# Kernel tuning notes

Measured on AMD Instinct MI355X. Metric: run time of the kernel, lower is better.

The kernel has to match this reference:

```python
import jax, jax.numpy as jnp
import numpy as np
from functools import partial

NPOINT, NSAMPLE = 1024, 32
EPS = 1e-5

def setup_inputs() -> dict:
    key = jax.random.key(0)
    ks = jax.random.split(key, 16)
    B, N, C = 16, 4096, 64
    d = {
        "xyz": jax.random.normal(ks[0], (B, N, 3), jnp.float32),
        "points": jax.random.normal(ks[1], (B, N, C), jnp.float32),
    }
    chans = [67, 64, 64, 128]
    for i in range(3):
        cin, cout = chans[i], chans[i + 1]
        d[f"w{i+1}"] = jax.random.normal(ks[2 + i], (cout, cin), jnp.float32) * (1.0 / np.sqrt(cin))
        d[f"b{i+1}"] = jnp.zeros((cout,), jnp.float32)
        d[f"g{i+1}"] = jnp.ones((cout,), jnp.float32)
        d[f"be{i+1}"] = jnp.zeros((cout,), jnp.float32)
    return d

def farthest_point_sample(xyz, npoint):
    # xyz: (B, N, 3); deterministic start index 0 (torch code uses randint)
    B, N, _ = xyz.shape
    bidx = jnp.arange(B)

    def step(carry, _):
        distance, farthest = carry
        centroid = xyz[bidx, farthest]                       # (B, 3)
        dist = jnp.sum((xyz - centroid[:, None, :]) ** 2, -1)  # (B, N)
        distance = jnp.minimum(distance, dist)
        return (distance, jnp.argmax(distance, axis=1)), farthest

    init = (jnp.full((B, N), 1e10, xyz.dtype), jnp.zeros((B,), jnp.int32))
    _, centroids = jax.lax.scan(step, init, None, length=npoint)  # (npoint, B)
    return centroids.T                                            # (B, npoint)

def knn_group(nsample, xyz, new_xyz, points):
    # xyz: (B,N,3), new_xyz: (B,S,3), points: (B,N,C)
    # squared distances (same topk ordering as cdist)
    d2 = (jnp.sum(new_xyz ** 2, -1)[:, :, None]
          + jnp.sum(xyz ** 2, -1)[:, None, :]
          - 2.0 * jnp.einsum("bsd,bnd->bsn", new_xyz, xyz))     # (B,S,N)
    _, idx = jax.lax.top_k(-d2, nsample)                          # (B,S,K)

    gather = jax.vmap(lambda feats, i: feats[i])                  # per-batch fancy index
    grouped_xyz = gather(xyz, idx) - new_xyz[:, :, None, :]       # (B,S,K,3)
    grouped_pts = jnp.concatenate([grouped_xyz, gather(points, idx)], -1)  # (B,S,K,3+C)
    return grouped_xyz, grouped_pts

def mlp_layer(x, w, b, g, be):
    # 1x1 conv + BatchNorm (batch stats, training mode) + ReLU
    y = jnp.einsum("bskc,oc->bsko", x, w) + b
    mu = jnp.mean(y, axis=(0, 1, 2))
    var = jnp.var(y, axis=(0, 1, 2))
    y = (y - mu) * jax.lax.rsqrt(var + EPS) * g + be
    return jax.nn.relu(y)

def reference(xyz, points, w1, b1, g1, be1, w2, b2, g2, be2, w3, b3, g3, be3):
    centroids = farthest_point_sample(xyz, NPOINT)                    # (B,S)
    new_xyz = jnp.take_along_axis(xyz, centroids[:, :, None], axis=1)  # (B,S,3)
    _, x = knn_group(NSAMPLE, xyz, new_xyz, points)                   # (B,S,K,3+C)
    x = mlp_layer(x, w1, b1, g1, be1)
    x = mlp_layer(x, w2, b2, g2, be2)
    x = mlp_layer(x, w3, b3, g3, be3)
    new_points = jnp.max(x, axis=2)                                   # (B,S,mlp[-1])
    return new_xyz, new_points
```

## Files before the change

### kernel.cpp

```cpp
#include <hip/hip_runtime.h>

typedef unsigned int   uint;
typedef unsigned short ushort;
typedef unsigned long long u64;
typedef float f32x4 __attribute__((ext_vector_type(4)));
typedef short bf16x8 __attribute__((ext_vector_type(8)));
typedef uint  uint2v __attribute__((ext_vector_type(2)));

#define STR 88

__device__ __forceinline__ uint packbf2(float a, float b){
  uint ua=__float_as_uint(a); ua=(ua+0x7fffu+((ua>>16)&1u))>>16;
  uint ub=__float_as_uint(b); ub=(ub+0x7fffu+((ub>>16)&1u))>>16;
  return ua|(ub<<16);
}
__device__ __forceinline__ ushort bf1(float a){
  uint ua=__float_as_uint(a); return (ushort)((ua+0x7fffu+((ua>>16)&1u))>>16);
}

__device__ __forceinline__ void dot16x2(const float* __restrict__ wr,
                                        const f32x4* xa, const f32x4* xb,
                                        float& accA, float& accB){
#pragma unroll
  for (int k=0;k<4;k++){
    f32x4 w=*(const f32x4*)(wr+4*k);
    accA=fmaf(xa[k][0],w[0],accA); accA=fmaf(xa[k][1],w[1],accA);
    accA=fmaf(xa[k][2],w[2],accA); accA=fmaf(xa[k][3],w[3],accA);
    accB=fmaf(xb[k][0],w[0],accB); accB=fmaf(xb[k][1],w[1],accB);
    accB=fmaf(xb[k][2],w[2],accB); accB=fmaf(xb[k][3],w[3],accB);
  }
}

__global__ __launch_bounds__(256) void k_fps(const float* __restrict__ xyz,
                                             int* __restrict__ cent,
                                             float* __restrict__ oxyz){
  __shared__ __align__(16) float sp[4096][4];
  __shared__ u64 rk[2][4];
  __shared__ int sel[1024];
  const int b = blockIdx.x, tid = threadIdx.x, lane=tid&63, wave=tid>>6;
  const float* xb = xyz + (long)b*4096*3;
  float px[16], py[16], pz[16], pd[16];
#pragma unroll
  for (int j=0;j<16;j++){
    int n = tid + 256*j;
    float x=xb[n*3], y=xb[n*3+1], z=xb[n*3+2];
    sp[n][0]=x; sp[n][1]=y; sp[n][2]=z; sp[n][3]=0.0f;
    px[j]=x; py[j]=y; pz[j]=z; pd[j]=1e10f;
  }
  if (tid==0) sel[0]=0;
  __syncthreads();
  int f = 0;
  for (int t=1;t<1024;t++){
    f32x4 c = *(const f32x4*)sp[f];
    float bv=-1.0f; int bi=0;
#pragma unroll
    for (int j=0;j<16;j++){
      int n = tid + 256*j;
      float dx=px[j]-c[0], dy=py[j]-c[1], dz=pz[j]-c[2];
      float d=__fadd_rn(__fadd_rn(__fmul_rn(dx,dx),__fmul_rn(dy,dy)),__fmul_rn(dz,dz));
      float mn=fminf(pd[j],d); pd[j]=mn;
      if (j==0){ bv=mn; bi=n; }
      else if (mn>bv){ bv=mn; bi=n; }
    }
    u64 key = ((u64)__float_as_uint(bv)<<32) | (uint)(~bi);
#pragma unroll
    for (int off=32;off;off>>=1){
      u64 ok=__shfl_xor(key,off);
      key = ok>key ? ok : key;
    }
    int par=t&1;
    if (lane==0) rk[par][wave]=key;
    __syncthreads();
    {
      u64 k0=rk[par][0], k1=rk[par][1], k2=rk[par][2], k3=rk[par][3];
      u64 ka = k0>k1?k0:k1;
      u64 kb = k2>k3?k2:k3;
      u64 kk = ka>kb?ka:kb;
      f = (int)(~(uint)kk) & 4095;
    }
    if (tid==0) sel[t]=f;
  }
  __syncthreads();
#pragma unroll
  for (int j=0;j<4;j++){
    int s = tid + 256*j;
    int n = sel[s];
    cent[b*1024+s]=n;
    f32x4 cf=*(const f32x4*)sp[n];
    oxyz[(b*1024+s)*3+0]=cf[0];
    oxyz[(b*1024+s)*3+1]=cf[1];
    oxyz[(b*1024+s)*3+2]=cf[2];
  }
}

__global__ __launch_bounds__(256) void k_knn(const float* __restrict__ xyz,
                                             const int* __restrict__ cent,
                                             ushort* __restrict__ kidx){
  __shared__ float sx[4096], sy[4096], sz[4096];
  const int bx=blockIdx.x, b=bx>>5, chunk=bx&31;
  const int tid=threadIdx.x, lane=tid&63, wave=tid>>6;
  const float* xb = xyz + (long)b*4096*3;
#pragma unroll
  for (int j=0;j<16;j++){
    int n = tid + 256*j;
    sx[n]=xb[n*3]; sy[n]=xb[n*3+1]; sz[n]=xb[n*3+2];
  }
  __syncthreads();
  const u64 SENT=~0ull;
  for (int qp=0; qp<4; qp++){
    int sA = chunk*32 + wave*8 + qp*2;
    int sB = sA + 1;
    int qnA = cent[b*1024 + sA] & 4095;
    int qnB = cent[b*1024 + sB] & 4095;
    double qxA=(double)sx[qnA], qyA=(double)sy[qnA], qzA=(double)sz[qnA];
    double qxB=(double)sx[qnB], qyB=(double)sy[qnB], qzB=(double)sz[qnB];
    u64 k1A=SENT, k2A=SENT, k1B=SENT, k2B=SENT;
#pragma unroll 4
    for (int j=0;j<64;j++){
      int n = lane + 64*j;
      double px=(double)sx[n], py=(double)sy[n], pz=(double)sz[n];
      double dxA=px-qxA, dyA=py-qyA, dzA=pz-qzA;
      double dxB=px-qxB, dyB=py-qyB, dzB=pz-qzB;
      double d2A = dxA*dxA + dyA*dyA + dzA*dzA;
      double d2B = dxB*dxB + dyB*dyB + dzB*dzB;
      u64 kdA = (((u64)__double_as_longlong(d2A)) & ~4095ull) | (uint)n;
      u64 kdB = (((u64)__double_as_longlong(d2B)) & ~4095ull) | (uint)n;
      if (kdA<k1A){ k2A=k1A; k1A=kdA; }
      else if (kdA<k2A){ k2A=kdA; }
      if (kdB<k1B){ k2B=k1B; k1B=kdB; }
      else if (kdB<k2B){ k2B=kdB; }
    }
    u64 removedA=0ull, removedB=0ull;
    ushort* outA = kidx + (b*1024 + sA)*32;
    ushort* outB = kidx + (b*1024 + sB)*32;
    for (int r=0;r<32;r++){
      u64 wkA=k1A, wkB=k1B;
#pragma unroll
      for (int off=32;off;off>>=1){
        u64 okA=__shfl_xor(wkA,off);
        u64 okB=__shfl_xor(wkB,off);
        wkA = okA<wkA ? okA : wkA;
        wkB = okB<wkB ? okB : wkB;
      }
      if (lane==0){ outA[r]=(ushort)(wkA & 4095u); outB[r]=(ushort)(wkB & 4095u); }
      if (wkA==k1A){
        removedA |= 1ull << (((uint)(k1A&4095u))>>6);
        if (k2A!=SENT){ k1A=k2A; k2A=SENT; }
        else {
          k1A=SENT; k2A=SENT;
#pragma unroll 4
          for (int j=0;j<64;j++){
            if ((removedA>>j)&1ull) continue;
            int n = lane + 64*j;
            double dx=(double)sx[n]-qxA, dy=(double)sy[n]-qyA, dz=(double)sz[n]-qzA;
            double d2 = dx*dx + dy*dy + dz*dz;
            u64 kd = (((u64)__double_as_longlong(d2)) & ~4095ull) | (uint)n;
            if (kd<k1A){ k2A=k1A; k1A=kd; }
            else if (kd<k2A){ k2A=kd; }
          }
        }
      }
      if (wkB==k1B){
        removedB |= 1ull << (((uint)(k1B&4095u))>>6);
        if (k2B!=SENT){ k1B=k2B; k2B=SENT; }
        else {
          k1B=SENT; k2B=SENT;
#pragma unroll 4
          for (int j=0;j<64;j++){
            if ((removedB>>j)&1ull) continue;
            int n = lane + 64*j;
            double dx=(double)sx[n]-qxB, dy=(double)sy[n]-qyB, dz=(double)sz[n]-qzB;
            double d2 = dx*dx + dy*dy + dz*dz;
            u64 kd = (((u64)__double_as_longlong(d2)) & ~4095ull) | (uint)n;
            if (kd<k1B){ k2B=k1B; k1B=kd; }
            else if (kd<k2B){ k2B=kd; }
          }
        }
      }
    }
  }
}

__global__ __launch_bounds__(256) void k_mlp1b(const float* __restrict__ xyz,
                                               const float* __restrict__ pts,
                                               const float* __restrict__ w1,
                                               const float* __restrict__ b1,
                                               const int* __restrict__ cent,
                                               const ushort* __restrict__ kidx,
                                               float* __restrict__ part,
                                               float* __restrict__ y){
  __shared__ __align__(16) float L[9760];
  float* W1  = L;
  float* XIN = L+4384;
  float* WRED= L+8736;
  const int tid=threadIdx.x, bi=blockIdx.x;
  const int row=tid>>3, oc=tid&7, wave=tid>>6;
  const int b=bi>>6, s0=(bi&63)*16;
  const long bN=(long)b*4096;

  for (int i=tid;i<64*68;i+=256){
    int r=i/68, c=i-r*68;
    float v = (c<64)? w1[r*67+3+c] : (c<67? w1[r*67+(c-64)] : 0.0f);
    W1[r*68+((r>>3)<<2)+c]=v;
  }
  float breg1[8];
#pragma unroll
  for (int i=0;i<8;i++) breg1[i]=b1[oc*8+i];
  float ps[8], pq[8];
#pragma unroll
  for (int s=0;s<8;s++){ ps[s]=0.f; pq[s]=0.f; }
  __syncthreads();

  for (int t=0; t<8; t++){
    int sgA = b*1024 + s0 + t*2, sgB = sgA+1;
    {
      int nA = kidx[sgA*32+row] & 4095;
      int nB = kidx[sgB*32+row] & 4095;
      const float* prA = pts + (bN+nA)*64;
      const float* prB = pts + (bN+nB)*64;
      *(f32x4*)(XIN + row*68 + oc*8)          = *(const f32x4*)(prA + oc*8);
      *(f32x4*)(XIN + row*68 + oc*8 + 4)      = *(const f32x4*)(prA + oc*8 + 4);
      *(f32x4*)(XIN + (row+32)*68 + oc*8)     = *(const f32x4*)(prB + oc*8);
      *(f32x4*)(XIN + (row+32)*68 + oc*8 + 4) = *(const f32x4*)(prB + oc*8 + 4);
      if (oc==0){
        int qA = cent[sgA] & 4095, qB = cent[sgB] & 4095;
        const float* xpA = xyz + (bN+nA)*3; const float* qpA = xyz + (bN+qA)*3;
        const float* xpB = xyz + (bN+nB)*3; const float* qpB = xyz + (bN+qB)*3;
        XIN[row*68+64]=xpA[0]-qpA[0]; XIN[row*68+65]=xpA[1]-qpA[1];
        XIN[row*68+66]=xpA[2]-qpA[2]; XIN[row*68+67]=0.0f;
        XIN[(row+32)*68+64]=xpB[0]-qpB[0]; XIN[(row+32)*68+65]=xpB[1]-qpB[1];
        XIN[(row+32)*68+66]=xpB[2]-qpB[2]; XIN[(row+32)*68+67]=0.0f;
      }
    }
    const float* xrowA = XIN + row*68;
    const float* xrowB = XIN + (row+32)*68;
    float acc[2][8];
#pragma unroll
    for (int i=0;i<8;i++){ acc[0][i]=breg1[i]; acc[1][i]=breg1[i]; }
#pragma unroll
    for (int co=0;co<4;co++){
      f32x4 xa[4], xbv[4];
#pragma unroll
      for (int k=0;k<4;k++){ xa[k]=*(const f32x4*)(xrowA+co*16+4*k); xbv[k]=*(const f32x4*)(xrowB+co*16+4*k); }
#pragma unroll
      for (int i=0;i<8;i++)
        dot16x2(W1+(oc*8+i)*68+(oc<<2)+co*16, xa, xbv, acc[0][i], acc[1][i]);
    }
    {
      f32x4 xtA=*(const f32x4*)(xrowA+64), xtB=*(const f32x4*)(xrowB+64);
#pragma unroll
      for (int i=0;i<8;i++){
        const float* wr=W1+(oc*8+i)*68+(oc<<2)+64;
        f32x4 w=*(const f32x4*)wr;
        acc[0][i]=fmaf(xtA[0],w[0],acc[0][i]); acc[0][i]=fmaf(xtA[1],w[1],acc[0][i]);
        acc[0][i]=fmaf(xtA[2],w[2],acc[0][i]); acc[0][i]=fmaf(xtA[3],w[3],acc[0][i]);
        acc[1][i]=fmaf(xtB[0],w[0],acc[1][i]); acc[1][i]=fmaf(xtB[1],w[1],acc[1][i]);
        acc[1][i]=fmaf(xtB[2],w[2],acc[1][i]); acc[1][i]=fmaf(xtB[3],w[3],acc[1][i]);
      }
    }
    {
      long baseA = ((long)sgA*32+row)*64 + oc*8;
      long baseB = ((long)sgB*32+row)*64 + oc*8;
      *(f32x4*)(y+baseA)   = (f32x4){acc[0][0],acc[0][1],acc[0][2],acc[0][3]};
      *(f32x4*)(y+baseA+4) = (f32x4){acc[0][4],acc[0][5],acc[0][6],acc[0][7]};
      *(f32x4*)(y+baseB)   = (f32x4){acc[1][0],acc[1][1],acc[1][2],acc[1][3]};
      *(f32x4*)(y+baseB+4) = (f32x4){acc[1][4],acc[1][5],acc[1][6],acc[1][7]};
    }
#pragma unroll
    for (int i=0;i<8;i++){
      ps[i]+=acc[0][i]+acc[1][i];
      pq[i]=fmaf(acc[0][i],acc[0][i],pq[i]); pq[i]=fmaf(acc[1][i],acc[1][i],pq[i]);
    }
  }
#pragma unroll
  for (int s=0;s<8;s++){
    ps[s]+=__shfl_xor(ps[s],8); ps[s]+=__shfl_xor(ps[s],16); ps[s]+=__shfl_xor(ps[s],32);
    pq[s]+=__shfl_xor(pq[s],8); pq[s]+=__shfl_xor(pq[s],16); pq[s]+=__shfl_xor(pq[s],32);
  }
  __syncthreads();
  if ((tid&63)<8){
    for (int s=0;s<8;s++){
      WRED[((wave*8+oc)*16+s)*2+0]=ps[s];
      WRED[((wave*8+oc)*16+s)*2+1]=pq[s];
    }
  }
  __syncthreads();
  if (tid<64){
    int o=tid, occ=o>>3, i=o&7;
    float s=0.f,q=0.f;
#pragma unroll
    for (int w=0;w<4;w++){ s+=WRED[((w*8+occ)*16+i)*2]; q+=WRED[((w*8+occ)*16+i)*2+1]; }
    part[(bi*64+o)*2]=s; part[(bi*64+o)*2+1]=q;
  }
}


__global__ __launch_bounds__(256) void k_mlp2m(const float* __restrict__ w2,
                                               const float* __restrict__ b2,
                                               const float* __restrict__ ab1,
                                               float* __restrict__ part,
                                               float* __restrict__ y){
  __shared__ __align__(16) ushort SA[128*STR];
  __shared__ __align__(16) ushort SW[64*STR];
  __shared__ float WRED[4*4*16*2];
  const int tid=threadIdx.x, bi=blockIdx.x;
  const int lane=tid&63, wave=tid>>6;
  const int lo16=lane&15, hi16=lane>>4;

  for (int i=tid;i<4096;i+=256){
    int r=i>>6, c=i&63;
    SW[r*STR+c]=bf1(w2[i]);
  }
  const int ch4=(tid&15)*4, rb=(tid>>4)*8;
  float a1[4],c1[4];
#pragma unroll
  for(int j=0;j<4;j++){ a1[j]=ab1[(ch4+j)*2]; c1[j]=ab1[(ch4+j)*2+1]; }
  float bbn[4];
#pragma unroll
  for (int nf=0;nf<4;nf++) bbn[nf]=b2[nf*16+lo16];
  float pss[4]={0.f,0.f,0.f,0.f}, pqq[4]={0.f,0.f,0.f,0.f};

  for (int t=0;t<4;t++){
    const long row0=(long)bi*512 + t*128;
    __syncthreads();
#pragma unroll
    for(int rr=0;rr<8;rr++){
      int r=rb+rr;
      f32x4 v=*(const f32x4*)(y+(row0+r)*64+ch4);
      float x0=fmaxf(fmaf(a1[0],v[0],c1[0]),0.f);
      float x1=fmaxf(fmaf(a1[1],v[1],c1[1]),0.f);
      float x2=fmaxf(fmaf(a1[2],v[2],c1[2]),0.f);
      float x3=fmaxf(fmaf(a1[3],v[3],c1[3]),0.f);
      uint2v pk; pk[0]=packbf2(x0,x1); pk[1]=packbf2(x2,x3);
      *(uint2v*)(SA+r*STR+ch4)=pk;
    }
    __syncthreads();
    const int mt=wave*32;
    f32x4 acc[2][4];
#pragma unroll
    for(int mf=0;mf<2;mf++)
#pragma unroll
      for(int nf=0;nf<4;nf++) acc[mf][nf]=(f32x4){0.f,0.f,0.f,0.f};
#pragma unroll
    for (int ks=0; ks<2; ks++){
      bf16x8 a0=*(const bf16x8*)(SA+(mt+lo16)*STR    + ks*32 + hi16*8);
      bf16x8 a1f=*(const bf16x8*)(SA+(mt+16+lo16)*STR + ks*32 + hi16*8);
      bf16x8 b0=*(const bf16x8*)(SW+(lo16)*STR     + ks*32 + hi16*8);
      bf16x8 b1=*(const bf16x8*)(SW+(16+lo16)*STR  + ks*32 + hi16*8);
      bf16x8 b2f=*(const bf16x8*)(SW+(32+lo16)*STR + ks*32 + hi16*8);
      bf16x8 b3f=*(const bf16x8*)(SW+(48+lo16)*STR + ks*32 + hi16*8);
      acc[0][0]=__builtin_amdgcn_mfma_f32_16x16x32_bf16(a0 ,b0 ,acc[0][0],0,0,0);
      acc[0][1]=__builtin_amdgcn_mfma_f32_16x16x32_bf16(a0 ,b1 ,acc[0][1],0,0,0);
      acc[0][2]=__builtin_amdgcn_mfma_f32_16x16x32_bf16(a0 ,b2f,acc[0][2],0,0,0);
      acc[0][3]=__builtin_amdgcn_mfma_f32_16x16x32_bf16(a0 ,b3f,acc[0][3],0,0,0);
      acc[1][0]=__builtin_amdgcn_mfma_f32_16x16x32_bf16(a1f,b0 ,acc[1][0],0,0,0);
      acc[1][1]=__builtin_amdgcn_mfma_f32_16x16x32_bf16(a1f,b1 ,acc[1][1],0,0,0);
      acc[1][2]=__builtin_amdgcn_mfma_f32_16x16x32_bf16(a1f,b2f,acc[1][2],0,0,0);
      acc[1][3]=__builtin_amdgcn_mfma_f32_16x16x32_bf16(a1f,b3f,acc[1][3],0,0,0);
    }
#pragma unroll
    for (int nf=0;nf<4;nf++){
#pragma unroll
      for (int mf=0;mf<2;mf++)
#pragma unroll
        for (int reg=0;reg<4;reg++){
          float d=acc[mf][nf][reg]+bbn[nf];
          long rr=row0+mt+mf*16+hi16*4+reg;
          y[rr*64 + nf*16+lo16]=d;
          pss[nf]+=d; pqq[nf]=fmaf(d,d,pqq[nf]);
        }
    }
  }
#pragma unroll
  for (int nf=0;nf<4;nf++){
    pss[nf]+=__shfl_xor(pss[nf],16); pss[nf]+=__shfl_xor(pss[nf],32);
    pqq[nf]+=__shfl_xor(pqq[nf],16); pqq[nf]+=__shfl_xor(pqq[nf],32);
  }
  if (lane<16){
#pragma unroll
    for (int nf=0;nf<4;nf++){
      WRED[((wave*4+nf)*16+lane)*2+0]=pss[nf];
      WRED[((wave*4+nf)*16+lane)*2+1]=pqq[nf];
    }
  }
  __syncthreads();
  if (tid<64){
    int ch=tid, nf=ch>>4, ci=ch&15;
    float s=0.f,q=0.f;
#pragma unroll
    for (int w=0;w<4;w++){ s+=WRED[((w*4+nf)*16+ci)*2]; q+=WRED[((w*4+nf)*16+ci)*2+1]; }
    part[(bi*64+ch)*2]=s; part[(bi*64+ch)*2+1]=q;
  }
}

__global__ __launch_bounds__(256) void k_mlp3m(const float* __restrict__ w3,
                                               const float* __restrict__ b3,
                                               const float* __restrict__ ab2,
                                               float* __restrict__ part,
                                               const float* __restrict__ y,
                                               float* __restrict__ mx){
  __shared__ __align__(16) ushort SA[128*STR];
  __shared__ __align__(16) ushort SW[128*STR];
  __shared__ float WRED[4*8*16*2];
  const int tid=threadIdx.x, bi=blockIdx.x;
  const int lane=tid&63, wave=tid>>6;
  const int lo16=lane&15, hi16=lane>>4;

  for (int i=tid;i<8192;i+=256){
    int r=i>>6, c=i&63;
    SW[r*STR+c]=bf1(w3[i]);
  }
  const int ch4=(tid&15)*4, rb=(tid>>4)*8;
  float a2[4],c2[4];
#pragma unroll
  for(int j=0;j<4;j++){ a2[j]=ab2[(ch4+j)*2]; c2[j]=ab2[(ch4+j)*2+1]; }
  float bbn[8];
#pragma unroll
  for (int nf=0;nf<8;nf++) bbn[nf]=b3[nf*16+lo16];
  float pss[8], pqq[8];
#pragma unroll
  for (int nf=0;nf<8;nf++){ pss[nf]=0.f; pqq[nf]=0.f; }

  for (int t=0;t<4;t++){
    const long row0=(long)bi*512 + t*128;
    __syncthreads();
#pragma unroll
    for(int rr=0;rr<8;rr++){
      int r=rb+rr;
      f32x4 v=*(const f32x4*)(y+(row0+r)*64+ch4);
      float x0=fmaxf(fmaf(a2[0],v[0],c2[0]),0.f);
      float x1=fmaxf(fmaf(a2[1],v[1],c2[1]),0.f);
      float x2=fmaxf(fmaf(a2[2],v[2],c2[2]),0.f);
      float x3=fmaxf(fmaf(a2[3],v[3],c2[3]),0.f);
      uint2v pk; pk[0]=packbf2(x0,x1); pk[1]=packbf2(x2,x3);
      *(uint2v*)(SA+r*STR+ch4)=pk;
    }
    __syncthreads();
    const int mt=wave*32;
    f32x4 acc[2][8];
#pragma unroll
    for(int mf=0;mf<2;mf++)
#pragma unroll
      for(int nf=0;nf<8;nf++) acc[mf][nf]=(f32x4){0.f,0.f,0.f,0.f};
#pragma unroll
    for (int ks=0; ks<2; ks++){
      bf16x8 a0=*(const bf16x8*)(SA+(mt+lo16)*STR    + ks*32 + hi16*8);
      bf16x8 a1f=*(const bf16x8*)(SA+(mt+16+lo16)*STR + ks*32 + hi16*8);
#pragma unroll
      for (int nf=0;nf<8;nf++){
        bf16x8 bv=*(const bf16x8*)(SW+(nf*16+lo16)*STR + ks*32 + hi16*8);
        acc[0][nf]=__builtin_amdgcn_mfma_f32_16x16x32_bf16(a0 ,bv,acc[0][nf],0,0,0);
        acc[1][nf]=__builtin_amdgcn_mfma_f32_16x16x32_bf16(a1f,bv,acc[1][nf],0,0,0);
      }
    }
    float vmx[8];
#pragma unroll
    for (int nf=0;nf<8;nf++) vmx[nf]=-3.0e38f;
#pragma unroll
    for (int nf=0;nf<8;nf++){
#pragma unroll
      for (int mf=0;mf<2;mf++)
#pragma unroll
        for (int reg=0;reg<4;reg++){
          float d=acc[mf][nf][reg]+bbn[nf];
          pss[nf]+=d; pqq[nf]=fmaf(d,d,pqq[nf]);
          vmx[nf]=fmaxf(vmx[nf],d);
        }
    }
#pragma unroll
    for (int nf=0;nf<8;nf++){
      vmx[nf]=fmaxf(vmx[nf],__shfl_xor(vmx[nf],16));
      vmx[nf]=fmaxf(vmx[nf],__shfl_xor(vmx[nf],32));
    }
    {
      long sg = (long)bi*16 + t*4 + wave;
      if (lane<16){
#pragma unroll
        for (int nf=0;nf<8;nf++) mx[sg*128 + nf*16 + lane]=vmx[nf];
      }
    }
  }
#pragma unroll
  for (int nf=0;nf<8;nf++){
    pss[nf]+=__shfl_xor(pss[nf],16); pss[nf]+=__shfl_xor(pss[nf],32);
    pqq[nf]+=__shfl_xor(pqq[nf],16); pqq[nf]+=__shfl_xor(pqq[nf],32);
  }
  if (lane<16){
#pragma unroll
    for (int nf=0;nf<8;nf++){
      WRED[((wave*8+nf)*16+lane)*2+0]=pss[nf];
      WRED[((wave*8+nf)*16+lane)*2+1]=pqq[nf];
    }
  }
  __syncthreads();
  if (tid<128){
    int ch=tid, nf=ch>>4, ci=ch&15;
    float s=0.f,q=0.f;
#pragma unroll
    for (int w=0;w<4;w++){ s+=WRED[((w*8+nf)*16+ci)*2]; q+=WRED[((w*8+nf)*16+ci)*2+1]; }
    part[(bi*128+ch)*2]=s; part[(bi*128+ch)*2+1]=q;
  }
}

__global__ void k_red(const float* __restrict__ part,
                      const float* __restrict__ gam,
                      const float* __restrict__ bet,
                      float* __restrict__ ab, int nch, int nblk){
  __shared__ float red[4][128][2];
  const int tid=threadIdx.x, ch=tid%nch, seg=tid/nch;
  float s=0.f,q=0.f;
  for (int i=seg;i<nblk;i+=4){ s+=part[(i*nch+ch)*2]; q+=part[(i*nch+ch)*2+1]; }
  red[seg][ch][0]=s; red[seg][ch][1]=q;
  __syncthreads();
  if (seg==0){
    s=red[0][ch][0]+red[1][ch][0]+red[2][ch][0]+red[3][ch][0];
    q=red[0][ch][1]+red[1][ch][1]+red[2][ch][1]+red[3][ch][1];
    float mu=s*(1.0f/524288.0f);
    float var=q*(1.0f/524288.0f)-mu*mu;
    var=fmaxf(var,0.0f);
    float a=gam[ch]/sqrtf(var+1e-5f);
    float c=bet[ch]-mu*a;
    ab[ch*2]=a; ab[ch*2+1]=c;
  }
}

__global__ __launch_bounds__(256) void k_out(const float* __restrict__ mx,
                                             const float* __restrict__ ab3,
                                             float* __restrict__ onp){
  int i = (blockIdx.x*256 + threadIdx.x)*4;
  int ch = i & 127;
  f32x4 v = *(const f32x4*)(mx+i);
  f32x4 r;
  r[0]=fmaxf(fmaf(ab3[(ch+0)*2], v[0], ab3[(ch+0)*2+1]), 0.0f);
  r[1]=fmaxf(fmaf(ab3[(ch+1)*2], v[1], ab3[(ch+1)*2+1]), 0.0f);
  r[2]=fmaxf(fmaf(ab3[(ch+2)*2], v[2], ab3[(ch+2)*2+1]), 0.0f);
  r[3]=fmaxf(fmaf(ab3[(ch+3)*2], v[3], ab3[(ch+3)*2+1]), 0.0f);
  *(f32x4*)(onp+i)=r;
}

extern "C" void kernel_launch(void* const* d_in, const int* in_sizes, int n_in,
                              void* d_out, int out_size, void* d_ws, size_t ws_size,
                              hipStream_t stream){
  const float* xyz=(const float*)d_in[0];
  const float* pts=(const float*)d_in[1];
  const float* w1 =(const float*)d_in[2];
  const float* b1 =(const float*)d_in[3];
  const float* g1 =(const float*)d_in[4];
  const float* be1=(const float*)d_in[5];
  const float* w2 =(const float*)d_in[6];
  const float* b2 =(const float*)d_in[7];
  const float* g2 =(const float*)d_in[8];
  const float* be2=(const float*)d_in[9];
  const float* w3 =(const float*)d_in[10];
  const float* b3 =(const float*)d_in[11];
  const float* g3 =(const float*)d_in[12];
  const float* be3=(const float*)d_in[13];
  char* ws=(char*)d_ws;
  int*    cent=(int*)(ws);
  ushort* kidx=(ushort*)(ws+  65536);
  float*  p   =(float*)(ws+ 1114112);
  float*  ab1 =(float*)(ws+ 2162688);
  float*  ab2 =(float*)(ws+ 2163200);
  float*  ab3 =(float*)(ws+ 2163712);
  float*  mx  =(float*)(ws+ 2164736);
  float*  y   =(float*)(ws+16777216);
  float* oxyz=(float*)d_out;
  float* onp =oxyz + 16*1024*3;

  k_fps<<<16, 256, 0, stream>>>(xyz, cent, oxyz);
  k_knn<<<512, 256, 0, stream>>>(xyz, cent, kidx);
  k_mlp1b<<<1024, 256, 0, stream>>>(xyz, pts, w1, b1, cent, kidx, p, y);
  k_red<<<1, 256, 0, stream>>>(p, g1, be1, ab1, 64, 1024);
  k_mlp2m<<<1024, 256, 0, stream>>>(w2, b2, ab1, p, y);
  k_red<<<1, 256, 0, stream>>>(p, g2, be2, ab2, 64, 1024);
  k_mlp3m<<<1024, 256, 0, stream>>>(w3, b3, ab2, p, y, mx);
  k_red<<<1, 512, 0, stream>>>(p, g3, be3, ab3, 128, 1024);
  k_out<<<2048, 256, 0, stream>>>(mx, ab3, onp);
}
```

Measured before the change: 1.741 ms.

## Rewrite first MLP layer with bf16 MFMA matrix instructions

Replaces the fp32 FMA-based first 1x1 conv kernel with one that converts gathered point features, relative xyz and weights to bf16 in shared memory. The K dimension is padded to 96 and the product is computed with 16x16x32 bf16 MFMA instructions, following the scheme already used by layers 2 and 3. This moves the layer-1 matmul off the vector ALUs onto the matrix cores. In exchange, inputs and weights are rounded to bf16, and outputs are written as strided scalar stores rather than vector stores.

```diff
diff --git a/kernel.cpp b/kernel.cpp
--- a/kernel.cpp
+++ b/kernel.cpp
@@ -7,7 +7,8 @@
 typedef short bf16x8 __attribute__((ext_vector_type(8)));
 typedef uint  uint2v __attribute__((ext_vector_type(2)));
 
-#define STR 88
+#define STR  88
+#define STR1 104
 
 __device__ __forceinline__ uint packbf2(float a, float b){
   uint ua=__float_as_uint(a); ua=(ua+0x7fffu+((ua>>16)&1u))>>16;
@@ -16,19 +17,6 @@
 }
 __device__ __forceinline__ ushort bf1(float a){
   uint ua=__float_as_uint(a); return (ushort)((ua+0x7fffu+((ua>>16)&1u))>>16);
-}
-
-__device__ __forceinline__ void dot16x2(const float* __restrict__ wr,
-                                        const f32x4* xa, const f32x4* xb,
-                                        float& accA, float& accB){
-#pragma unroll
-  for (int k=0;k<4;k++){
-    f32x4 w=*(const f32x4*)(wr+4*k);
-    accA=fmaf(xa[k][0],w[0],accA); accA=fmaf(xa[k][1],w[1],accA);
-    accA=fmaf(xa[k][2],w[2],accA); accA=fmaf(xa[k][3],w[3],accA);
-    accB=fmaf(xb[k][0],w[0],accB); accB=fmaf(xb[k][1],w[1],accB);
-    accB=fmaf(xb[k][2],w[2],accB); accB=fmaf(xb[k][3],w[3],accB);
-  }
 }
 
 __global__ __launch_bounds__(256) void k_fps(const float* __restrict__ xyz,
@@ -181,7 +169,8 @@
   }
 }
 
-__global__ __launch_bounds__(256) void k_mlp1b(const float* __restrict__ xyz,
+
+__global__ __launch_bounds__(256) void k_mlp1m(const float* __restrict__ xyz,
                                                const float* __restrict__ pts,
                                                const float* __restrict__ w1,
                                                const float* __restrict__ b1,
@@ -189,111 +178,110 @@
                                                const ushort* __restrict__ kidx,
                                                float* __restrict__ part,
                                                float* __restrict__ y){
-  __shared__ __align__(16) float L[9760];
-  float* W1  = L;
-  float* XIN = L+4384;
-  float* WRED= L+8736;
+  __shared__ __align__(16) ushort SA[128*STR1];
+  __shared__ __align__(16) ushort SW[64*STR1];
+  __shared__ float WRED[4*4*16*2];
   const int tid=threadIdx.x, bi=blockIdx.x;
-  const int row=tid>>3, oc=tid&7, wave=tid>>6;
-  const int b=bi>>6, s0=(bi&63)*16;
-  const long bN=(long)b*4096;
-
-  for (int i=tid;i<64*68;i+=256){
-    int r=i/68, c=i-r*68;
+  const int lane=tid&63, wave=tid>>6;
+  const int lo16=lane&15, hi16=lane>>4;
+  const long bN=(long)(bi>>6)*4096;
+
+  for (int i=tid;i<64*96;i+=256){
+    int r=i/96, c=i-r*96;
     float v = (c<64)? w1[r*67+3+c] : (c<67? w1[r*67+(c-64)] : 0.0f);
-    W1[r*68+((r>>3)<<2)+c]=v;
-  }
-  float breg1[8];
-#pragma unroll
-  for (int i=0;i<8;i++) breg1[i]=b1[oc*8+i];
-  float ps[8], pq[8];
-#pragma unroll
-  for (int s=0;s<8;s++){ ps[s]=0.f; pq[s]=0.f; }
-  __syncthreads();
-
-  for (int t=0; t<8; t++){
-    int sgA = b*1024 + s0 + t*2, sgB = sgA+1;
-    {
-      int nA = kidx[sgA*32+row] & 4095;
-      int nB = kidx[sgB*32+row] & 4095;
-      const float* prA = pts + (bN+nA)*64;
-      const float* prB = pts + (bN+nB)*64;
-      *(f32x4*)(XIN + row*68 + oc*8)          = *(const f32x4*)(prA + oc*8);
-      *(f32x4*)(XIN + row*68 + oc*8 + 4)      = *(const f32x4*)(prA + oc*8 + 4);
-      *(f32x4*)(XIN + (row+32)*68 + oc*8)     = *(const f32x4*)(prB + oc*8);
-      *(f32x4*)(XIN + (row+32)*68 + oc*8 + 4) = *(const f32x4*)(prB + oc*8 + 4);
-      if (oc==0){
-        int qA = cent[sgA] & 4095, qB = cent[sgB] & 4095;
-        const float* xpA = xyz + (bN+nA)*3; const float* qpA = xyz + (bN+qA)*3;
-        const float* xpB = xyz + (bN+nB)*3; const float* qpB = xyz + (bN+qB)*3;
-        XIN[row*68+64]=xpA[0]-qpA[0]; XIN[row*68+65]=xpA[1]-qpA[1];
-        XIN[row*68+66]=xpA[2]-qpA[2]; XIN[row*68+67]=0.0f;
-        XIN[(row+32)*68+64]=xpB[0]-qpB[0]; XIN[(row+32)*68+65]=xpB[1]-qpB[1];
-        XIN[(row+32)*68+66]=xpB[2]-qpB[2]; XIN[(row+32)*68+67]=0.0f;
-      }
-    }
-    const float* xrowA = XIN + row*68;
-    const float* xrowB = XIN + (row+32)*68;
-    float acc[2][8];
-#pragma unroll
-    for (int i=0;i<8;i++){ acc[0][i]=breg1[i]; acc[1][i]=breg1[i]; }
-#pragma unroll
-    for (int co=0;co<4;co++){
-      f32x4 xa[4], xbv[4];
-#pragma unroll
-      for (int k=0;k<4;k++){ xa[k]=*(const f32x4*)(xrowA+co*16+4*k); xbv[k]=*(const f32x4*)(xrowB+co*16+4*k); }
-#pragma unroll
-      for (int i=0;i<8;i++)
-        dot16x2(W1+(oc*8+i)*68+(oc<<2)+co*16, xa, xbv, acc[0][i], acc[1][i]);
-    }
-    {
-      f32x4 xtA=*(const f32x4*)(xrowA+64), xtB=*(const f32x4*)(xrowB+64);
-#pragma unroll
-      for (int i=0;i<8;i++){
-        const float* wr=W1+(oc*8+i)*68+(oc<<2)+64;
-        f32x4 w=*(const f32x4*)wr;
-        acc[0][i]=fmaf(xtA[0],w[0],acc[0][i]); acc[0][i]=fmaf(xtA[1],w[1],acc[0][i]);
-        acc[0][i]=fmaf(xtA[2],w[2],acc[0][i]); acc[0][i]=fmaf(xtA[3],w[3],acc[0][i]);
-        acc[1][i]=fmaf(xtB[0],w[0],acc[1][i]); acc[1][i]=fmaf(xtB[1],w[1],acc[1][i]);
-        acc[1][i]=fmaf(xtB[2],w[2],acc[1][i]); acc[1][i]=fmaf(xtB[3],w[3],acc[1][i]);
-      }
-    }
-    {
-      long baseA = ((long)sgA*32+row)*64 + oc*8;
-      long baseB = ((long)sgB*32+row)*64 + oc*8;
-      *(f32x4*)(y+baseA)   = (f32x4){acc[0][0],acc[0][1],acc[0][2],acc[0][3]};
-      *(f32x4*)(y+baseA+4) = (f32x4){acc[0][4],acc[0][5],acc[0][6],acc[0][7]};
-      *(f32x4*)(y+baseB)   = (f32x4){acc[1][0],acc[1][1],acc[1][2],acc[1][3]};
-      *(f32x4*)(y+baseB+4) = (f32x4){acc[1][4],acc[1][5],acc[1][6],acc[1][7]};
-    }
-#pragma unroll
-    for (int i=0;i<8;i++){
-      ps[i]+=acc[0][i]+acc[1][i];
-      pq[i]=fmaf(acc[0][i],acc[0][i],pq[i]); pq[i]=fmaf(acc[1][i],acc[1][i],pq[i]);
-    }
-  }
-#pragma unroll
-  for (int s=0;s<8;s++){
-    ps[s]+=__shfl_xor(ps[s],8); ps[s]+=__shfl_xor(ps[s],16); ps[s]+=__shfl_xor(ps[s],32);
-    pq[s]+=__shfl_xor(pq[s],8); pq[s]+=__shfl_xor(pq[s],16); pq[s]+=__shfl_xor(pq[s],32);
-  }
-  __syncthreads();
-  if ((tid&63)<8){
-    for (int s=0;s<8;s++){
-      WRED[((wave*8+oc)*16+s)*2+0]=ps[s];
-      WRED[((wave*8+oc)*16+s)*2+1]=pq[s];
+    SW[r*STR1+c]=bf1(v);
+  }
+  for (int i=tid;i<128*32;i+=256){
+    int r=i>>5, c=64+(i&31);
+    SA[r*STR1+c]=0;
+  }
+  const int ch4=(tid&15)*4, rb=(tid>>4)*8;
+  float a1r[4];
+#pragma unroll
+  for (int nf=0;nf<4;nf++) a1r[nf]=b1[nf*16+lo16];
+  float pss[4]={0.f,0.f,0.f,0.f}, pqq[4]={0.f,0.f,0.f,0.f};
+
+  for (int t=0;t<4;t++){
+    const long row0=(long)bi*512 + t*128;
+    __syncthreads();
+#pragma unroll
+    for(int rr=0;rr<8;rr++){
+      int r=rb+rr;
+      long grow=row0+r;
+      int n = kidx[grow] & 4095;
+      f32x4 v=*(const f32x4*)(pts + (bN+n)*64 + ch4);
+      uint2v pk; pk[0]=packbf2(v[0],v[1]); pk[1]=packbf2(v[2],v[3]);
+      *(uint2v*)(SA+r*STR1+ch4)=pk;
+    }
+    if (tid<128){
+      int r=tid;
+      long grow=row0+r;
+      int n = kidx[grow] & 4095;
+      int q = cent[grow>>5] & 4095;
+      const float* xp = xyz + (bN+n)*3;
+      const float* qp = xyz + (bN+q)*3;
+      SA[r*STR1+64]=bf1(xp[0]-qp[0]);
+      SA[r*STR1+65]=bf1(xp[1]-qp[1]);
+      SA[r*STR1+66]=bf1(xp[2]-qp[2]);
+    }
+    __syncthreads();
+    const int mt=wave*32;
+    f32x4 acc[2][4];
+#pragma unroll
+    for(int mf=0;mf<2;mf++)
+#pragma unroll
+      for(int nf=0;nf<4;nf++) acc[mf][nf]=(f32x4){0.f,0.f,0.f,0.f};
+#pragma unroll
+    for (int ks=0; ks<3; ks++){
+      bf16x8 a0=*(const bf16x8*)(SA+(mt+lo16)*STR1    + ks*32 + hi16*8);
+      bf16x8 a1f=*(const bf16x8*)(SA+(mt+16+lo16)*STR1 + ks*32 + hi16*8);
+      bf16x8 b0=*(const bf16x8*)(SW+(lo16)*STR1     + ks*32 + hi16*8);
+      bf16x8 b1f=*(const bf16x8*)(SW+(16+lo16)*STR1 + ks*32 + hi16*8);
+      bf16x8 b2f=*(const bf16x8*)(SW+(32+lo16)*STR1 + ks*32 + hi16*8);
+      bf16x8 b3f=*(const bf16x8*)(SW+(48+lo16)*STR1 + ks*32 + hi16*8);
+      acc[0][0]=__builtin_amdgcn_mfma_f32_16x16x32_bf16(a0 ,b0 ,acc[0][0],0,0,0);
+      acc[0][1]=__builtin_amdgcn_mfma_f32_16x16x32_bf16(a0 ,b1f,acc[0][1],0,0,0);
+      acc[0][2]=__builtin_amdgcn_mfma_f32_16x16x32_bf16(a0 ,b2f,acc[0][2],0,0,0);
+      acc[0][3]=__builtin_amdgcn_mfma_f32_16x16x32_bf16(a0 ,b3f,acc[0][3],0,0,0);
+      acc[1][0]=__builtin_amdgcn_mfma_f32_16x16x32_bf16(a1f,b0 ,acc[1][0],0,0,0);
+      acc[1][1]=__builtin_amdgcn_mfma_f32_16x16x32_bf16(a1f,b1f,acc[1][1],0,0,0);
+      acc[1][2]=__builtin_amdgcn_mfma_f32_16x16x32_bf16(a1f,b2f,acc[1][2],0,0,0);
+      acc[1][3]=__builtin_amdgcn_mfma_f32_16x16x32_bf16(a1f,b3f,acc[1][3],0,0,0);
+    }
+#pragma unroll
+    for (int nf=0;nf<4;nf++){
+#pragma unroll
+      for (int mf=0;mf<2;mf++)
+#pragma unroll
+        for (int reg=0;reg<4;reg++){
+          float d=acc[mf][nf][reg]+a1r[nf];
+          long rr=row0+mt+mf*16+hi16*4+reg;
+          y[rr*64 + nf*16+lo16]=d;
+          pss[nf]+=d; pqq[nf]=fmaf(d,d,pqq[nf]);
+        }
+    }
+  }
+#pragma unroll
+  for (int nf=0;nf<4;nf++){
+    pss[nf]+=__shfl_xor(pss[nf],16); pss[nf]+=__shfl_xor(pss[nf],32);
+    pqq[nf]+=__shfl_xor(pqq[nf],16); pqq[nf]+=__shfl_xor(pqq[nf],32);
+  }
+  if (lane<16){
+#pragma unroll
+    for (int nf=0;nf<4;nf++){
+      WRED[((wave*4+nf)*16+lane)*2+0]=pss[nf];
+      WRED[((wave*4+nf)*16+lane)*2+1]=pqq[nf];
     }
   }
   __syncthreads();
   if (tid<64){
-    int o=tid, occ=o>>3, i=o&7;
+    int ch=tid, nf=ch>>4, ci=ch&15;
     float s=0.f,q=0.f;
 #pragma unroll
-    for (int w=0;w<4;w++){ s+=WRED[((w*8+occ)*16+i)*2]; q+=WRED[((w*8+occ)*16+i)*2+1]; }
-    part[(bi*64+o)*2]=s; part[(bi*64+o)*2+1]=q;
-  }
-}
-
+    for (int w=0;w<4;w++){ s+=WRED[((w*4+nf)*16+ci)*2]; q+=WRED[((w*4+nf)*16+ci)*2+1]; }
+    part[(bi*64+ch)*2]=s; part[(bi*64+ch)*2+1]=q;
+  }
+}
 
 __global__ __launch_bounds__(256) void k_mlp2m(const float* __restrict__ w2,
                                                const float* __restrict__ b2,
@@ -569,7 +557,7 @@
 
   k_fps<<<16, 256, 0, stream>>>(xyz, cent, oxyz);
   k_knn<<<512, 256, 0, stream>>>(xyz, cent, kidx);
-  k_mlp1b<<<1024, 256, 0, stream>>>(xyz, pts, w1, b1, cent, kidx, p, y);
+  k_mlp1m<<<1024, 256, 0, stream>>>(xyz, pts, w1, b1, cent, kidx, p, y);
   k_red<<<1, 256, 0, stream>>>(p, g1, be1, ab1, 64, 1024);
   k_mlp2m<<<1024, 256, 0, stream>>>(w2, b2, ab1, p, y);
   k_red<<<1, 256, 0, stream>>>(p, g2, be2, ab2, 64, 1024);
```

After: 1.700 ms. 2.4% less time.
